# Kernel tuning notes

Hardware: AMD Instinct MI355X
Metric: run time of the kernel (lower is better)

Reference implementation:

```python
import jax, jax.numpy as jnp
import numpy as np

MAX_NORM = 20.0
V, D, B, L, K = 100000, 64, 4096, 50, 3


def setup_inputs() -> dict:
    key = jax.random.key(0)
    k0, k1, k2, k3 = jax.random.split(key, 4)
    embeddings = jax.random.normal(k0, (V, D), dtype=jnp.float32)
    tokens_l = jax.random.randint(k1, (B, L), 0, V)
    tokens_r = jax.random.randint(k2, (B, L), 0, V)
    tokens_neg = jax.random.randint(k3, (B, K, L), 0, V)
    return {"embeddings": embeddings, "tokens_l": tokens_l,
            "tokens_r": tokens_r, "tokens_neg": tokens_neg}


def _renorm(w):
    # nn.Embedding(max_norm=20): rows with norm > max_norm are rescaled to max_norm
    norms = jnp.linalg.norm(w, axis=1, keepdims=True)
    scale = jnp.where(norms > MAX_NORM, MAX_NORM / norms, 1.0)
    return w * scale


def _embed_bag(w, tokens):
    # gather rows then sum-pool over the last (token) axis -> embedding-bag 'sum'
    return jnp.take(w, tokens, axis=0).sum(axis=-2)


def reference(embeddings, tokens_l, tokens_r, tokens_neg):
    w = _renorm(embeddings)
    l_batch = _embed_bag(w, tokens_l)[:, None, :]     # [B, 1, D]
    r_batch = _embed_bag(w, tokens_r)[:, None, :]     # [B, 1, D]
    neg_batch = _embed_bag(w, tokens_neg)             # [B, K, D]
    return (l_batch, r_batch, neg_batch)
```

## Files before the change

kernel.cpp:

```cpp
#include <hip/hip_runtime.h>
#include <math.h>

#define V_SZ 100000
#define D_SZ 64
#define B_SZ 4096
#define L_SZ 50
#define K_SZ 3
#define MAX_NORM 20.0f

__global__ __launch_bounds__(256) void fused_bag_kernel(
    const float* __restrict__ emb,
    const int* __restrict__ tl, const int* __restrict__ tr,
    const int* __restrict__ tn, float* __restrict__ out) {
    const int NBAGS = B_SZ * (2 + K_SZ);
    int wave = (int)((blockIdx.x * (unsigned)blockDim.x + threadIdx.x) >> 6);
    int lane = threadIdx.x & 63;
    if (wave >= NBAGS) return;

    const int* tok;
    if (wave < B_SZ)            tok = tl + (long)wave * L_SZ;
    else if (wave < 2 * B_SZ)   tok = tr + (long)(wave - B_SZ) * L_SZ;
    else                        tok = tn + (long)(wave - 2 * B_SZ) * L_SZ;

    int t = (lane < L_SZ) ? tok[lane] : 0;

    int m = lane & 15;
    int g = lane >> 4;

    float4 acc = make_float4(0.f, 0.f, 0.f, 0.f);

    #pragma unroll
    for (int i = 0; i < 13; ++i) {
        int j = i * 4 + g;
        int tj = __shfl(t, j, 64);
        const float4* row = (const float4*)(emb + (long)tj * D_SZ);
        float4 v = row[m];
        float ss = v.x * v.x + v.y * v.y + v.z * v.z + v.w * v.w;
        #pragma unroll
        for (int off = 1; off <= 8; off <<= 1)
            ss += __shfl_xor(ss, off, 16);
        float n = sqrtf(ss);
        float s = (n > MAX_NORM) ? (MAX_NORM / n) : 1.0f;
        s = (j < L_SZ) ? s : 0.0f;
        acc.x = fmaf(s, v.x, acc.x);
        acc.y = fmaf(s, v.y, acc.y);
        acc.z = fmaf(s, v.z, acc.z);
        acc.w = fmaf(s, v.w, acc.w);
    }

    #pragma unroll
    for (int off = 16; off <= 32; off <<= 1) {
        acc.x += __shfl_xor(acc.x, off, 64);
        acc.y += __shfl_xor(acc.y, off, 64);
        acc.z += __shfl_xor(acc.z, off, 64);
        acc.w += __shfl_xor(acc.w, off, 64);
    }
    if (g == 0) {
        float4* o = (float4*)(out + (long)wave * D_SZ);
        o[m] = acc;
    }
}

extern "C" void kernel_launch(void* const* d_in, const int* in_sizes, int n_in,
                              void* d_out, int out_size, void* d_ws, size_t ws_size,
                              hipStream_t stream) {
    const float* emb = (const float*)d_in[0];
    const int* tl = (const int*)d_in[1];
    const int* tr = (const int*)d_in[2];
    const int* tn = (const int*)d_in[3];
    float* out = (float*)d_out;
    (void)d_ws; (void)ws_size;

    const int NBAGS = B_SZ * (2 + K_SZ);
    int grid = NBAGS / 4;
    fused_bag_kernel<<<grid, 256, 0, stream>>>(emb, tl, tr, tn, out);
}
```

Before: 104.4 us.

## Pre-renormalize embedding table into fp16 workspace, then gather half-precision rows

```diff
diff --git a/kernel.cpp b/kernel.cpp
--- a/kernel.cpp
+++ b/kernel.cpp
@@ -1,4 +1,5 @@
 #include <hip/hip_runtime.h>
+#include <hip/hip_fp16.h>
 #include <math.h>
 
 #define V_SZ 100000
@@ -8,8 +9,27 @@
 #define K_SZ 3
 #define MAX_NORM 20.0f
 
-__global__ __launch_bounds__(256) void fused_bag_kernel(
-    const float* __restrict__ emb,
+__global__ __launch_bounds__(256) void renorm_fp16_kernel(
+    const float* __restrict__ emb, __half* __restrict__ tab) {
+    int row = blockIdx.x * 16 + (threadIdx.x >> 4);
+    int m = threadIdx.x & 15;
+    if (row >= V_SZ) return;
+    const float4* row4 = (const float4*)(emb + (long)row * D_SZ);
+    float4 v = row4[m];
+    float ss = v.x * v.x + v.y * v.y + v.z * v.z + v.w * v.w;
+    #pragma unroll
+    for (int off = 1; off <= 8; off <<= 1)
+        ss += __shfl_xor(ss, off, 16);
+    float n = sqrtf(ss);
+    float s = (n > MAX_NORM) ? (MAX_NORM / n) : 1.0f;
+    union { int2 i2; __half2 h[2]; } u;
+    u.h[0] = __floats2half2_rn(s * v.x, s * v.y);
+    u.h[1] = __floats2half2_rn(s * v.z, s * v.w);
+    ((int2*)(tab + (long)row * D_SZ))[m] = u.i2;
+}
+
+__global__ __launch_bounds__(256) void embed_bag_fp16_kernel(
+    const __half* __restrict__ tab,
     const int* __restrict__ tl, const int* __restrict__ tr,
     const int* __restrict__ tn, float* __restrict__ out) {
     const int NBAGS = B_SZ * (2 + K_SZ);
@@ -28,24 +48,19 @@
     int g = lane >> 4;
 
     float4 acc = make_float4(0.f, 0.f, 0.f, 0.f);
-
     #pragma unroll
     for (int i = 0; i < 13; ++i) {
         int j = i * 4 + g;
         int tj = __shfl(t, j, 64);
-        const float4* row = (const float4*)(emb + (long)tj * D_SZ);
-        float4 v = row[m];
-        float ss = v.x * v.x + v.y * v.y + v.z * v.z + v.w * v.w;
-        #pragma unroll
-        for (int off = 1; off <= 8; off <<= 1)
-            ss += __shfl_xor(ss, off, 16);
-        float n = sqrtf(ss);
-        float s = (n > MAX_NORM) ? (MAX_NORM / n) : 1.0f;
-        s = (j < L_SZ) ? s : 0.0f;
-        acc.x = fmaf(s, v.x, acc.x);
-        acc.y = fmaf(s, v.y, acc.y);
-        acc.z = fmaf(s, v.z, acc.z);
-        acc.w = fmaf(s, v.w, acc.w);
+        union { int2 i2; __half2 h[2]; } u;
+        u.i2 = ((const int2*)(tab + (long)tj * D_SZ))[m];
+        float2 f0 = __half22float2(u.h[0]);
+        float2 f1 = __half22float2(u.h[1]);
+        float s = (j < L_SZ) ? 1.0f : 0.0f;
+        acc.x = fmaf(s, f0.x, acc.x);
+        acc.y = fmaf(s, f0.y, acc.y);
+        acc.z = fmaf(s, f1.x, acc.z);
+        acc.w = fmaf(s, f1.y, acc.w);
     }
 
     #pragma unroll
@@ -69,9 +84,11 @@
     const int* tr = (const int*)d_in[2];
     const int* tn = (const int*)d_in[3];
     float* out = (float*)d_out;
-    (void)d_ws; (void)ws_size;
+    __half* tab = (__half*)d_ws;
+
+    renorm_fp16_kernel<<<(V_SZ + 15) / 16, 256, 0, stream>>>(emb, tab);
 
     const int NBAGS = B_SZ * (2 + K_SZ);
     int grid = NBAGS / 4;
-    fused_bag_kernel<<<grid, 256, 0, stream>>>(emb, tl, tr, tn, out);
+    embed_bag_fp16_kernel<<<grid, 256, 0, stream>>>(tab, tl, tr, tn, out);
 }
```

New measurement: 93.95 us. 10.0% less time.

## Prequantize renormalized table to int8 with per-row scale before gather

Applied to the files above, without the earlier changes.

```diff
diff --git a/kernel.cpp b/kernel.cpp
--- a/kernel.cpp
+++ b/kernel.cpp
@@ -8,8 +8,39 @@
 #define K_SZ 3
 #define MAX_NORM 20.0f
 
-__global__ __launch_bounds__(256) void fused_bag_kernel(
-    const float* __restrict__ emb,
+__global__ __launch_bounds__(256) void renorm_int8_kernel(
+    const float* __restrict__ emb, unsigned char* __restrict__ tab8,
+    float* __restrict__ invscale) {
+    int row = blockIdx.x * 16 + (threadIdx.x >> 4);
+    int m = threadIdx.x & 15;
+    if (row >= V_SZ) return;
+    const float4* row4 = (const float4*)(emb + (long)row * D_SZ);
+    float4 v = row4[m];
+    float ss = v.x * v.x + v.y * v.y + v.z * v.z + v.w * v.w;
+    float mx = fmaxf(fmaxf(fabsf(v.x), fabsf(v.y)), fmaxf(fabsf(v.z), fabsf(v.w)));
+    #pragma unroll
+    for (int off = 1; off <= 8; off <<= 1) {
+        ss += __shfl_xor(ss, off, 16);
+        mx = fmaxf(mx, __shfl_xor(mx, off, 16));
+    }
+    float n = sqrtf(ss);
+    float s = (n > MAX_NORM) ? (MAX_NORM / n) : 1.0f;
+    float rowmax = fmaxf(s * mx, 1e-20f);
+    float qs = 127.0f / rowmax;
+    int q0 = (int)rintf(s * v.x * qs) + 128;
+    int q1 = (int)rintf(s * v.y * qs) + 128;
+    int q2 = (int)rintf(s * v.z * qs) + 128;
+    int q3 = (int)rintf(s * v.w * qs) + 128;
+    unsigned int packed = (unsigned int)(q0 & 0xff) |
+                          ((unsigned int)(q1 & 0xff) << 8) |
+                          ((unsigned int)(q2 & 0xff) << 16) |
+                          ((unsigned int)(q3 & 0xff) << 24);
+    ((unsigned int*)(tab8 + (long)row * D_SZ))[m] = packed;
+    if (m == 0) invscale[row] = rowmax / 127.0f;
+}
+
+__global__ __launch_bounds__(256) void embed_bag_int8_kernel(
+    const unsigned char* __restrict__ tab8, const float* __restrict__ invscale,
     const int* __restrict__ tl, const int* __restrict__ tr,
     const int* __restrict__ tn, float* __restrict__ out) {
     const int NBAGS = B_SZ * (2 + K_SZ);
@@ -22,30 +53,27 @@
     else if (wave < 2 * B_SZ)   tok = tr + (long)(wave - B_SZ) * L_SZ;
     else                        tok = tn + (long)(wave - 2 * B_SZ) * L_SZ;
 
-    int t = (lane < L_SZ) ? tok[lane] : 0;
+    int   t  = (lane < L_SZ) ? tok[lane] : 0;
+    float sc = (lane < L_SZ) ? invscale[t] : 0.0f;
 
     int m = lane & 15;
     int g = lane >> 4;
 
     float4 acc = make_float4(0.f, 0.f, 0.f, 0.f);
-
     #pragma unroll
     for (int i = 0; i < 13; ++i) {
         int j = i * 4 + g;
-        int tj = __shfl(t, j, 64);
-        const float4* row = (const float4*)(emb + (long)tj * D_SZ);
-        float4 v = row[m];
-        float ss = v.x * v.x + v.y * v.y + v.z * v.z + v.w * v.w;
-        #pragma unroll
-        for (int off = 1; off <= 8; off <<= 1)
-            ss += __shfl_xor(ss, off, 16);
-        float n = sqrtf(ss);
-        float s = (n > MAX_NORM) ? (MAX_NORM / n) : 1.0f;
-        s = (j < L_SZ) ? s : 0.0f;
-        acc.x = fmaf(s, v.x, acc.x);
-        acc.y = fmaf(s, v.y, acc.y);
-        acc.z = fmaf(s, v.z, acc.z);
-        acc.w = fmaf(s, v.w, acc.w);
+        int   tj = __shfl(t, j, 64);
+        float sj = __shfl(sc, j, 64);
+        unsigned int u = ((const unsigned int*)(tab8 + (long)tj * D_SZ))[m];
+        float f0 = (float)( u        & 0xff) - 128.0f;
+        float f1 = (float)((u >> 8 ) & 0xff) - 128.0f;
+        float f2 = (float)((u >> 16) & 0xff) - 128.0f;
+        float f3 = (float)( u >> 24       ) - 128.0f;
+        acc.x = fmaf(sj, f0, acc.x);
+        acc.y = fmaf(sj, f1, acc.y);
+        acc.z = fmaf(sj, f2, acc.z);
+        acc.w = fmaf(sj, f3, acc.w);
     }
 
     #pragma unroll
@@ -69,9 +97,13 @@
     const int* tr = (const int*)d_in[2];
     const int* tn = (const int*)d_in[3];
     float* out = (float*)d_out;
-    (void)d_ws; (void)ws_size;
+
+    unsigned char* tab8 = (unsigned char*)d_ws;
+    float* invscale = (float*)(tab8 + (long)V_SZ * D_SZ);
+
+    renorm_int8_kernel<<<(V_SZ + 15) / 16, 256, 0, stream>>>(emb, tab8, invscale);
 
     const int NBAGS = B_SZ * (2 + K_SZ);
     int grid = NBAGS / 4;
-    fused_bag_kernel<<<grid, 256, 0, stream>>>(emb, tl, tr, tn, out);
+    embed_bag_int8_kernel<<<grid, 256, 0, stream>>>(tab8, invscale, tl, tr, tn, out);
 }
```

Result: faster. 92.78 us (-11.2%).
